# Optimization experiments

Measured on AMD Instinct MI355X. Metric: run time of the kernel, lower is better.

The kernel has to match this reference:

```python
import jax, jax.numpy as jnp
import numpy as np

N = 50000   # nodes per graph
D = 256     # embedding dim
E = 800000  # edges per graph
NEG_SLOPE = 0.2
EPS = 1e-9


def gat_layer(h, src, dst, W, a):
    # SpGraphAttentionLayer: transform, edge attention exp(-leakyrelu(a.[h_i||h_j])),
    # softmax-normalized scatter aggregation, ELU activation.
    h = h @ W                                   # [N, D]
    # a.[h_src || h_dst] == (h @ a[:D])[src] + (h @ a[D:])[dst]  (avoids [E,2D] concat)
    alpha_src = h @ a[:D]                       # [N]
    alpha_dst = h @ a[D:]                       # [N]
    logits = alpha_src[src] + alpha_dst[dst]    # [E]
    e = jnp.exp(-jax.nn.leaky_relu(logits, NEG_SLOPE))  # [E], pyGAT sparse form
    rowsum = jax.ops.segment_sum(e, src, num_segments=N)            # [N]
    num = jax.ops.segment_sum(e[:, None] * h[dst], src, num_segments=N)  # [N, D]
    out = num / (rowsum[:, None] + EPS)
    return jax.nn.elu(out)


def setup_inputs() -> dict:
    key = jax.random.key(0)
    ks = jax.random.split(key, 8)
    w_std = float(np.sqrt(2.0 / (D + D)))  # xavier
    sr_emb = jax.random.normal(ks[0], (N, D), jnp.float32) * w_std
    tg_emb = jax.random.normal(ks[1], (N, D), jnp.float32) * w_std
    W1 = jax.random.normal(ks[2], (D, D), jnp.float32) * w_std
    a1 = jax.random.normal(ks[3], (2 * D,), jnp.float32) * 0.1
    W2 = jax.random.normal(ks[4], (D, D), jnp.float32) * w_std
    a2 = jax.random.normal(ks[5], (2 * D,), jnp.float32) * 0.1
    adj_sr = jax.random.randint(ks[6], (2, E), 0, N, dtype=jnp.int64)
    adj_tg = jax.random.randint(ks[7], (2, E), 0, N, dtype=jnp.int64)
    return {"sr_emb": sr_emb, "tg_emb": tg_emb, "W1": W1, "a1": a1,
            "W2": W2, "a2": a2, "adj_sr": adj_sr, "adj_tg": adj_tg}


def reference(sr_emb, tg_emb, W1, a1, W2, a2, adj_sr, adj_tg):
    # layers are shared across the two graphs (same ModuleList applied to both)
    src_s, dst_s = adj_sr[0], adj_sr[1]
    src_t, dst_t = adj_tg[0], adj_tg[1]
    for (W, a) in ((W1, a1), (W2, a2)):
        sr_emb = gat_layer(sr_emb, src_s, dst_s, W, a)
        tg_emb = gat_layer(tg_emb, src_t, dst_t, W, a)
    return (sr_emb, tg_emb)
```

## Files before the change

kernel.cpp:

```cpp
#include <hip/hip_runtime.h>

#define NEG_SLOPE 0.2f
#define EPS_ 1e-9f

typedef __attribute__((ext_vector_type(8))) short short8v;
typedef __attribute__((ext_vector_type(4))) float f32x4;

__device__ __forceinline__ float bf2f(unsigned short u) {
    return __uint_as_float(((unsigned)u) << 16);
}
__device__ __forceinline__ unsigned short f2bf(float f) {
    unsigned u = __float_as_uint(f);
    u = u + 0x7FFFu + ((u >> 16) & 1u);
    return (unsigned short)(u >> 16);
}

__global__ void hist_kernel(const int* __restrict__ src, int* __restrict__ cnt, int E) {
    int i = blockIdx.x * blockDim.x + threadIdx.x;
    if (i < E) atomicAdd(&cnt[src[i]], 1);
}

__global__ __launch_bounds__(256) void scan1_kernel(const int* __restrict__ cnt,
        int* __restrict__ locpre, int* __restrict__ blocksum, int n) {
    int t = threadIdx.x;
    int lane = t & 63, wid = t >> 6;
    int base = blockIdx.x * 1024 + t * 4;
    int4 v = {0, 0, 0, 0};
    if (base + 3 < n) {
        v = *(const int4*)(cnt + base);
    } else {
        if (base + 0 < n) v.x = cnt[base + 0];
        if (base + 1 < n) v.y = cnt[base + 1];
        if (base + 2 < n) v.z = cnt[base + 2];
        if (base + 3 < n) v.w = cnt[base + 3];
    }
    int s = v.x + v.y + v.z + v.w;
    int incl = s;
    for (int off = 1; off < 64; off <<= 1) {
        int u = __shfl_up(incl, off);
        if (lane >= off) incl += u;
    }
    __shared__ int ws[4];
    if (lane == 63) ws[wid] = incl;
    __syncthreads();
    int woff = 0;
    for (int i = 0; i < wid; ++i) woff += ws[i];
    int excl = incl - s + woff;
    int4 o;
    o.x = excl; o.y = excl + v.x; o.z = o.y + v.y; o.w = o.z + v.z;
    if (base + 3 < n) {
        *(int4*)(locpre + base) = o;
    } else {
        if (base + 0 < n) locpre[base + 0] = o.x;
        if (base + 1 < n) locpre[base + 1] = o.y;
        if (base + 2 < n) locpre[base + 2] = o.z;
        if (base + 3 < n) locpre[base + 3] = o.w;
    }
    if (t == 255) blocksum[blockIdx.x] = excl + s;
}

__global__ __launch_bounds__(64) void scan2_kernel(int* __restrict__ blocksum, int nb,
        int* __restrict__ totout) {
    int lane = threadIdx.x;
    int carry = 0;
    for (int base = 0; base < nb; base += 64) {
        int v = (base + lane < nb) ? blocksum[base + lane] : 0;
        int incl = v;
        for (int off = 1; off < 64; off <<= 1) {
            int u = __shfl_up(incl, off);
            if (lane >= off) incl += u;
        }
        int tot = __shfl(incl, 63);
        if (base + lane < nb) blocksum[base + lane] = incl - v + carry;
        carry += tot;
    }
    if (lane == 0) *totout = carry;
}

__global__ __launch_bounds__(256) void scan3_kernel(const int* __restrict__ locpre,
        const int* __restrict__ blocksum, int* __restrict__ row_ptr,
        int* __restrict__ cursor, int n) {
    int base = blockIdx.x * 1024 + threadIdx.x * 4;
    int off = blocksum[blockIdx.x];
    if (base + 3 < n) {
        int4 v = *(const int4*)(locpre + base);
        v.x += off; v.y += off; v.z += off; v.w += off;
        *(int4*)(row_ptr + base) = v;
        *(int4*)(cursor + base) = v;
    } else {
        for (int i = 0; i < 4; ++i) {
            if (base + i < n) {
                int v = locpre[base + i] + off;
                row_ptr[base + i] = v;
                cursor[base + i] = v;
            }
        }
    }
}

__global__ void scatter_kernel(const int* __restrict__ src, const int* __restrict__ dst,
        int* __restrict__ cursor, int* __restrict__ colv, int* __restrict__ srce, int E) {
    int i = blockIdx.x * blockDim.x + threadIdx.x;
    if (i < E) {
        int s = src[i];
        int p = atomicAdd(&cursor[s], 1);
        colv[p] = dst[i];
        srce[p] = s;
    }
}

__global__ __launch_bounds__(256) void ew_kernel(const int* __restrict__ srce,
        const int* __restrict__ colv, const float* __restrict__ asrc,
        const float* __restrict__ adst, int2* __restrict__ ewc, int E) {
    int i = blockIdx.x * blockDim.x + threadIdx.x;
    if (i < E) {
        int d = colv[i];
        float x = asrc[srce[i]] + adst[d];
        float lr = fmaxf(x, NEG_SLOPE * x);
        ewc[i] = make_int2(d, __float_as_int(__expf(-lr)));
    }
}

__global__ void wt_kernel(const float* __restrict__ W, short* __restrict__ Wt) {
    int nn = blockIdx.x, k = threadIdx.x;
    Wt[nn * 256 + k] = (short)f2bf(W[k * 256 + nn]);
}

template<bool IN_BF16>
__global__ __launch_bounds__(256) void gemm_kernel(const void* __restrict__ hin,
        const short* __restrict__ Wt, unsigned short* __restrict__ hpS,
        const float* __restrict__ af, float* __restrict__ asrc,
        float* __restrict__ adst, int M) {
    __shared__ short As[64 * 40];
    __shared__ short Bt[256 * 40];
    int tid = threadIdx.x;
    int lane = tid & 63, w = tid >> 6;
    int m0 = blockIdx.x * 64;
    size_t Ns = (size_t)M * 32;

    f32x4 acc[16];
#pragma unroll
    for (int t = 0; t < 16; ++t) acc[t] = (f32x4){0.f, 0.f, 0.f, 0.f};

    int ar = tid >> 2;
    int ac = (tid & 3) * 8;
    int agrow = m0 + ar;

    for (int kk = 0; kk < 256; kk += 32) {
        short8v av = (short8v){0,0,0,0,0,0,0,0};
        if constexpr (IN_BF16) {
            if (agrow < M)
                av = *(const short8v*)((const short*)hin + (size_t)agrow * 256 + kk + ac);
        } else {
            if (agrow < M) {
                const float* s = (const float*)hin + (size_t)agrow * 256 + kk + ac;
                float4 v0 = *(const float4*)s;
                float4 v1 = *(const float4*)(s + 4);
                av[0] = (short)f2bf(v0.x); av[1] = (short)f2bf(v0.y);
                av[2] = (short)f2bf(v0.z); av[3] = (short)f2bf(v0.w);
                av[4] = (short)f2bf(v1.x); av[5] = (short)f2bf(v1.y);
                av[6] = (short)f2bf(v1.z); av[7] = (short)f2bf(v1.w);
            }
        }
        *(short8v*)&As[ar * 40 + ac] = av;
        {
            const short* s = Wt + (size_t)tid * 256 + kk;
#pragma unroll
            for (int i = 0; i < 4; ++i)
                *(short8v*)&Bt[tid * 40 + i * 8] = *(const short8v*)(s + i * 8);
        }
        __syncthreads();
        short8v a = *(const short8v*)&As[(16 * w + (lane & 15)) * 40 + (lane >> 4) * 8];
#pragma unroll
        for (int t = 0; t < 16; ++t) {
            short8v b = *(const short8v*)&Bt[(16 * t + (lane & 15)) * 40 + (lane >> 4) * 8];
            acc[t] = __builtin_amdgcn_mfma_f32_16x16x32_bf16(a, b, acc[t], 0, 0, 0);
        }
        __syncthreads();
    }
    int r0 = 16 * w + (lane >> 4) * 4;
    int c0 = lane & 15;
    float a_s[16], a_d[16];
#pragma unroll
    for (int t = 0; t < 16; ++t) {
        a_s[t] = af[16 * t + c0];
        a_d[t] = af[256 + 16 * t + c0];
    }
#pragma unroll
    for (int j = 0; j < 4; ++j) {
        int grow = m0 + r0 + j;
        float ssrc = 0.f, sdst = 0.f;
#pragma unroll
        for (int t = 0; t < 16; ++t) {
            float cv = acc[t][j];
            ssrc = fmaf(cv, a_s[t], ssrc);
            sdst = fmaf(cv, a_d[t], sdst);
            int col = 16 * t + c0;
            if (grow < M)
                hpS[(size_t)(col >> 5) * Ns + (size_t)grow * 32 + (col & 31)] = f2bf(cv);
        }
        for (int off = 1; off < 16; off <<= 1) {
            ssrc += __shfl_xor(ssrc, off);
            sdst += __shfl_xor(sdst, off);
        }
        if (c0 == 0 && grow < M) { asrc[grow] = ssrc; adst[grow] = sdst; }
    }
}

#define EWLD(pp, kk) int2 pp = ewc[min(e + kk, last)];
#define GA(qq, pp)   uint2 qq = *(const uint2*)(base + (size_t)(unsigned)pp.x * 32 + c4);
#define WSEL(ww, pp, kk) float ww = (kk < m) ? __int_as_float(pp.y) : 0.f;
#define ACC(qq, ww) { \
    acc0 = fmaf(ww, __uint_as_float(qq.x << 16), acc0); \
    acc1 = fmaf(ww, __uint_as_float(qq.x & 0xFFFF0000u), acc1); \
    acc2 = fmaf(ww, __uint_as_float(qq.y << 16), acc2); \
    acc3 = fmaf(ww, __uint_as_float(qq.y & 0xFFFF0000u), acc3); \
    rs += ww; }

template<bool OUT_BF16>
__global__ __launch_bounds__(256) void aggregate_kernel(const int* __restrict__ row_ptr,
        const int2* __restrict__ ewc, const unsigned short* __restrict__ hpS,
        void* __restrict__ outp, int n) {
    int bid = blockIdx.x;
    int slice = bid & 7;
    int wid = threadIdx.x >> 6;
    int lane = threadIdx.x & 63;
    int node = (bid >> 3) * 32 + wid * 8 + (lane >> 3);
    int c4 = (lane & 7) * 4;
    bool valid = node < n;
    int nd = valid ? node : 0;
    int beg = row_ptr[nd];
    int end = valid ? row_ptr[nd + 1] : beg;
    int last = end - 1;
    const unsigned short* __restrict__ base = hpS + (size_t)slice * ((size_t)n * 32);
    float acc0 = 0.f, acc1 = 0.f, acc2 = 0.f, acc3 = 0.f, rs = 0.f;
    for (int e = beg; e < end; e += 8) {
        int m = end - e;
        EWLD(p0, 0) EWLD(p1, 1) EWLD(p2, 2) EWLD(p3, 3)
        EWLD(p4, 4) EWLD(p5, 5) EWLD(p6, 6) EWLD(p7, 7)
        GA(q0, p0) GA(q1, p1) GA(q2, p2) GA(q3, p3)
        GA(q4, p4) GA(q5, p5) GA(q6, p6) GA(q7, p7)
        WSEL(w0, p0, 0) WSEL(w1, p1, 1) WSEL(w2, p2, 2) WSEL(w3, p3, 3)
        WSEL(w4, p4, 4) WSEL(w5, p5, 5) WSEL(w6, p6, 6) WSEL(w7, p7, 7)
        ACC(q0, w0) ACC(q1, w1) ACC(q2, w2) ACC(q3, w3)
        ACC(q4, w4) ACC(q5, w5) ACC(q6, w6) ACC(q7, w7)
    }
    if (valid) {
        float inv = 1.f / (rs + EPS_);
        float v0 = acc0 * inv, v1 = acc1 * inv, v2 = acc2 * inv, v3 = acc3 * inv;
        v0 = v0 > 0.f ? v0 : __expf(v0) - 1.f;
        v1 = v1 > 0.f ? v1 : __expf(v1) - 1.f;
        v2 = v2 > 0.f ? v2 : __expf(v2) - 1.f;
        v3 = v3 > 0.f ? v3 : __expf(v3) - 1.f;
        size_t o = (size_t)node * 256 + slice * 32 + c4;
        if constexpr (OUT_BF16) {
            ushort4 ov;
            ov.x = f2bf(v0); ov.y = f2bf(v1); ov.z = f2bf(v2); ov.w = f2bf(v3);
            *(ushort4*)((unsigned short*)outp + o) = ov;
        } else {
            float4 ov = {v0, v1, v2, v3};
            *(float4*)((float*)outp + o) = ov;
        }
    }
}

extern "C" void kernel_launch(void* const* d_in, const int* in_sizes, int n_in,
                              void* d_out, int out_size, void* d_ws, size_t ws_size,
                              hipStream_t stream) {
    const float* sr_emb = (const float*)d_in[0];
    const float* tg_emb = (const float*)d_in[1];
    const float* W1 = (const float*)d_in[2];
    const float* a1 = (const float*)d_in[3];
    const float* W2 = (const float*)d_in[4];
    const float* a2 = (const float*)d_in[5];
    const int* adj_sr = (const int*)d_in[6];
    const int* adj_tg = (const int*)d_in[7];
    int N = in_sizes[0] / 256;
    int E = in_sizes[6] / 2;

    char* p = (char*)d_ws;
    auto alloc = [&](size_t bytes) -> void* {
        void* r = (void*)p;
        p += (bytes + 255) & ~(size_t)255;
        return r;
    };
    int nb = (N + 1023) / 1024;
    int* cnt      = (int*)alloc((size_t)N * 4);
    int* row_ptr  = (int*)alloc((size_t)(N + 1) * 4);
    int* cursor   = (int*)alloc((size_t)N * 4);
    int* locpre   = (int*)alloc((size_t)N * 4);
    int* blocksum = (int*)alloc((size_t)nb * 4);
    int* colv     = (int*)alloc((size_t)(E + 16) * 4);
    int* srce     = (int*)alloc((size_t)(E + 16) * 4);
    int2* ewc     = (int2*)alloc((size_t)(E + 16) * 8);
    short* Wt1    = (short*)alloc(256 * 256 * 2);
    short* Wt2    = (short*)alloc(256 * 256 * 2);
    unsigned short* hpS = (unsigned short*)alloc((size_t)N * 256 * 2);
    float* asrc   = (float*)alloc((size_t)N * 4);
    float* adst   = (float*)alloc((size_t)N * 4);
    short* tmp    = (short*)alloc((size_t)N * 256 * 2);

    wt_kernel<<<256, 256, 0, stream>>>(W1, Wt1);
    wt_kernel<<<256, 256, 0, stream>>>(W2, Wt2);

    int gemm_grid = (N + 63) / 64;
    int agg_grid = 8 * ((N + 31) / 32);
    int e_grid = (E + 255) / 256;

    for (int g = 0; g < 2; ++g) {
        const int* srcv = (g == 0 ? adj_sr : adj_tg);
        const int* dstv = srcv + E;
        const float* emb = (g == 0 ? sr_emb : tg_emb);
        float* outg = (float*)d_out + (size_t)g * N * 256;

        hipMemsetAsync(cnt, 0, (size_t)N * 4, stream);
        hist_kernel<<<e_grid, 256, 0, stream>>>(srcv, cnt, E);
        scan1_kernel<<<nb, 256, 0, stream>>>(cnt, locpre, blocksum, N);
        scan2_kernel<<<1, 64, 0, stream>>>(blocksum, nb, row_ptr + N);
        scan3_kernel<<<nb, 256, 0, stream>>>(locpre, blocksum, row_ptr, cursor, N);
        scatter_kernel<<<e_grid, 256, 0, stream>>>(srcv, dstv, cursor, colv, srce, E);

        gemm_kernel<false><<<gemm_grid, 256, 0, stream>>>(emb, Wt1, hpS, a1, asrc, adst, N);
        ew_kernel<<<e_grid, 256, 0, stream>>>(srce, colv, asrc, adst, ewc, E);
        aggregate_kernel<true><<<agg_grid, 256, 0, stream>>>(row_ptr, ewc, hpS, tmp, N);
        gemm_kernel<true><<<gemm_grid, 256, 0, stream>>>(tmp, Wt2, hpS, a2, asrc, adst, N);
        ew_kernel<<<e_grid, 256, 0, stream>>>(srce, colv, asrc, adst, ewc, E);
        aggregate_kernel<false><<<agg_grid, 256, 0, stream>>>(row_ptr, ewc, hpS, outg, N);
    }
}
```

Measured before the change: 671.8 us.

## Batch both graphs per launch, fuse edge weights into aggregation, split alpha

Processes both graphs in each kernel launch via a grid dimension, which halves the launch count and fills the GPU better. Edge attention weights are computed inside the aggregation from colv, asrc and adst, so the separate ew_kernel and its int2 edge buffer (and srce) are gone. The GEMM is rewritten to stage half of W in LDS once and hold the A fragments in registers, and the alpha dot-products move to a separate kernel that rereads hpS. The layer-1 output is stored as fp32 in the output buffer rather than a bf16 temporary, which adds memory traffic, and the bf16 exp work now repeats per feature slice.

```diff
diff --git a/kernel.cpp b/kernel.cpp
--- a/kernel.cpp
+++ b/kernel.cpp
@@ -15,24 +15,32 @@
     return (unsigned short)(u >> 16);
 }
 
-__global__ void hist_kernel(const int* __restrict__ src, int* __restrict__ cnt, int E) {
+__global__ void hist_kernel(const int* __restrict__ srcA, const int* __restrict__ srcB,
+        int* __restrict__ cnt, int E, int n) {
+    int g = blockIdx.y;
+    const int* src = g ? srcB : srcA;
+    int* c = cnt + (size_t)g * n;
     int i = blockIdx.x * blockDim.x + threadIdx.x;
-    if (i < E) atomicAdd(&cnt[src[i]], 1);
+    if (i < E) atomicAdd(&c[src[i]], 1);
 }
 
 __global__ __launch_bounds__(256) void scan1_kernel(const int* __restrict__ cnt,
-        int* __restrict__ locpre, int* __restrict__ blocksum, int n) {
+        int* __restrict__ locpre, int* __restrict__ blocksum, int n, int nb) {
+    int g = blockIdx.y;
+    const int* cg = cnt + (size_t)g * n;
+    int* lg = locpre + (size_t)g * n;
+    int* bs = blocksum + (size_t)g * nb;
     int t = threadIdx.x;
     int lane = t & 63, wid = t >> 6;
     int base = blockIdx.x * 1024 + t * 4;
     int4 v = {0, 0, 0, 0};
     if (base + 3 < n) {
-        v = *(const int4*)(cnt + base);
+        v = *(const int4*)(cg + base);
     } else {
-        if (base + 0 < n) v.x = cnt[base + 0];
-        if (base + 1 < n) v.y = cnt[base + 1];
-        if (base + 2 < n) v.z = cnt[base + 2];
-        if (base + 3 < n) v.w = cnt[base + 3];
+        if (base + 0 < n) v.x = cg[base + 0];
+        if (base + 1 < n) v.y = cg[base + 1];
+        if (base + 2 < n) v.z = cg[base + 2];
+        if (base + 3 < n) v.w = cg[base + 3];
     }
     int s = v.x + v.y + v.z + v.w;
     int incl = s;
@@ -49,75 +57,74 @@
     int4 o;
     o.x = excl; o.y = excl + v.x; o.z = o.y + v.y; o.w = o.z + v.z;
     if (base + 3 < n) {
-        *(int4*)(locpre + base) = o;
+        *(int4*)(lg + base) = o;
     } else {
-        if (base + 0 < n) locpre[base + 0] = o.x;
-        if (base + 1 < n) locpre[base + 1] = o.y;
-        if (base + 2 < n) locpre[base + 2] = o.z;
-        if (base + 3 < n) locpre[base + 3] = o.w;
-    }
-    if (t == 255) blocksum[blockIdx.x] = excl + s;
+        if (base + 0 < n) lg[base + 0] = o.x;
+        if (base + 1 < n) lg[base + 1] = o.y;
+        if (base + 2 < n) lg[base + 2] = o.z;
+        if (base + 3 < n) lg[base + 3] = o.w;
+    }
+    if (t == 255) bs[blockIdx.x] = excl + s;
 }
 
 __global__ __launch_bounds__(64) void scan2_kernel(int* __restrict__ blocksum, int nb,
-        int* __restrict__ totout) {
+        int* __restrict__ row_ptr, int n) {
+    int g = blockIdx.y;
+    int* bs = blocksum + (size_t)g * nb;
     int lane = threadIdx.x;
     int carry = 0;
     for (int base = 0; base < nb; base += 64) {
-        int v = (base + lane < nb) ? blocksum[base + lane] : 0;
+        int v = (base + lane < nb) ? bs[base + lane] : 0;
         int incl = v;
         for (int off = 1; off < 64; off <<= 1) {
             int u = __shfl_up(incl, off);
             if (lane >= off) incl += u;
         }
         int tot = __shfl(incl, 63);
-        if (base + lane < nb) blocksum[base + lane] = incl - v + carry;
+        if (base + lane < nb) bs[base + lane] = incl - v + carry;
         carry += tot;
     }
-    if (lane == 0) *totout = carry;
+    if (lane == 0) row_ptr[(size_t)g * (n + 1) + n] = carry;
 }
 
 __global__ __launch_bounds__(256) void scan3_kernel(const int* __restrict__ locpre,
         const int* __restrict__ blocksum, int* __restrict__ row_ptr,
-        int* __restrict__ cursor, int n) {
+        int* __restrict__ cursor, int n, int nb) {
+    int g = blockIdx.y;
+    const int* lg = locpre + (size_t)g * n;
+    const int* bs = blocksum + (size_t)g * nb;
+    int* rp = row_ptr + (size_t)g * (n + 1);
+    int* cu = cursor + (size_t)g * n;
     int base = blockIdx.x * 1024 + threadIdx.x * 4;
-    int off = blocksum[blockIdx.x];
+    int off = bs[blockIdx.x];
     if (base + 3 < n) {
-        int4 v = *(const int4*)(locpre + base);
+        int4 v = *(const int4*)(lg + base);
         v.x += off; v.y += off; v.z += off; v.w += off;
-        *(int4*)(row_ptr + base) = v;
-        *(int4*)(cursor + base) = v;
+        *(int4*)(rp + base) = v;
+        *(int4*)(cu + base) = v;
     } else {
         for (int i = 0; i < 4; ++i) {
             if (base + i < n) {
-                int v = locpre[base + i] + off;
-                row_ptr[base + i] = v;
-                cursor[base + i] = v;
+                int v = lg[base + i] + off;
+                rp[base + i] = v;
+                cu[base + i] = v;
             }
         }
     }
 }
 
-__global__ void scatter_kernel(const int* __restrict__ src, const int* __restrict__ dst,
-        int* __restrict__ cursor, int* __restrict__ colv, int* __restrict__ srce, int E) {
+__global__ void scatter_kernel(const int* __restrict__ srcA, const int* __restrict__ dstA,
+        const int* __restrict__ srcB, const int* __restrict__ dstB,
+        int* __restrict__ cursor, int* __restrict__ colv, int E, int n, int ecap) {
+    int g = blockIdx.y;
+    const int* src = g ? srcB : srcA;
+    const int* dst = g ? dstB : dstA;
+    int* cu = cursor + (size_t)g * n;
+    int* cv = colv + (size_t)g * ecap;
     int i = blockIdx.x * blockDim.x + threadIdx.x;
     if (i < E) {
-        int s = src[i];
-        int p = atomicAdd(&cursor[s], 1);
-        colv[p] = dst[i];
-        srce[p] = s;
-    }
-}
-
-__global__ __launch_bounds__(256) void ew_kernel(const int* __restrict__ srce,
-        const int* __restrict__ colv, const float* __restrict__ asrc,
-        const float* __restrict__ adst, int2* __restrict__ ewc, int E) {
-    int i = blockIdx.x * blockDim.x + threadIdx.x;
-    if (i < E) {
-        int d = colv[i];
-        float x = asrc[srce[i]] + adst[d];
-        float lr = fmaxf(x, NEG_SLOPE * x);
-        ewc[i] = make_int2(d, __float_as_int(__expf(-lr)));
+        int p = atomicAdd(&cu[src[i]], 1);
+        cv[p] = dst[i];
     }
 }
 
@@ -126,90 +133,137 @@
     Wt[nn * 256 + k] = (short)f2bf(W[k * 256 + nn]);
 }
 
-template<bool IN_BF16>
-__global__ __launch_bounds__(256) void gemm_kernel(const void* __restrict__ hin,
-        const short* __restrict__ Wt, unsigned short* __restrict__ hpS,
-        const float* __restrict__ af, float* __restrict__ asrc,
-        float* __restrict__ adst, int M) {
-    __shared__ short As[64 * 40];
-    __shared__ short Bt[256 * 40];
+__global__ __launch_bounds__(512) void gemm_kernel(const float* __restrict__ hinA,
+        const float* __restrict__ hinB, const short* __restrict__ Wt,
+        unsigned short* __restrict__ hpS_all, int M) {
+    __shared__ short Bt[32768];
     int tid = threadIdx.x;
     int lane = tid & 63, w = tid >> 6;
-    int m0 = blockIdx.x * 64;
+    int ch = blockIdx.y;
+    int g = blockIdx.z;
+    const float* hin = g ? hinB : hinA;
+    unsigned short* hpS = hpS_all + (size_t)g * M * 256;
+
+    {
+        int n = tid >> 2;
+        int kb = (tid & 3) * 64;
+        const short* srcw = Wt + (size_t)(ch * 128 + n) * 256;
+#pragma unroll
+        for (int i = 0; i < 8; ++i) {
+            int k = kb + i * 8;
+            short8v v = *(const short8v*)(srcw + k);
+            *(short8v*)&Bt[((k >> 3) * 128 + n) * 8] = v;
+        }
+    }
+    __syncthreads();
+
+    int row0 = (blockIdx.x * 8 + w) * 16;
+    if (row0 >= M) return;
+
+    const float* Ap = hin + (size_t)(row0 + (lane & 15)) * 256 + (lane >> 4) * 8;
+    short8v af[8];
+#pragma unroll
+    for (int half = 0; half < 2; ++half) {
+        float4 u0[4], u1[4];
+#pragma unroll
+        for (int c = 0; c < 4; ++c) {
+            u0[c] = *(const float4*)(Ap + (half * 4 + c) * 32);
+            u1[c] = *(const float4*)(Ap + (half * 4 + c) * 32 + 4);
+        }
+#pragma unroll
+        for (int c = 0; c < 4; ++c) {
+            short8v a;
+            a[0] = (short)f2bf(u0[c].x); a[1] = (short)f2bf(u0[c].y);
+            a[2] = (short)f2bf(u0[c].z); a[3] = (short)f2bf(u0[c].w);
+            a[4] = (short)f2bf(u1[c].x); a[5] = (short)f2bf(u1[c].y);
+            a[6] = (short)f2bf(u1[c].z); a[7] = (short)f2bf(u1[c].w);
+            af[half * 4 + c] = a;
+        }
+    }
+
+    f32x4 acc[8];
+#pragma unroll
+    for (int t = 0; t < 8; ++t) acc[t] = (f32x4){0.f, 0.f, 0.f, 0.f};
+
+#pragma unroll
+    for (int c = 0; c < 8; ++c) {
+        int kcf = c * 4 + (lane >> 4);
+#pragma unroll
+        for (int t = 0; t < 8; ++t) {
+            short8v b = *(const short8v*)&Bt[(kcf * 128 + t * 16 + (lane & 15)) * 8];
+            acc[t] = __builtin_amdgcn_mfma_f32_16x16x32_bf16(af[c], b, acc[t], 0, 0, 0);
+        }
+    }
+
     size_t Ns = (size_t)M * 32;
-
-    f32x4 acc[16];
-#pragma unroll
-    for (int t = 0; t < 16; ++t) acc[t] = (f32x4){0.f, 0.f, 0.f, 0.f};
-
-    int ar = tid >> 2;
-    int ac = (tid & 3) * 8;
-    int agrow = m0 + ar;
-
-    for (int kk = 0; kk < 256; kk += 32) {
-        short8v av = (short8v){0,0,0,0,0,0,0,0};
-        if constexpr (IN_BF16) {
-            if (agrow < M)
-                av = *(const short8v*)((const short*)hin + (size_t)agrow * 256 + kk + ac);
-        } else {
-            if (agrow < M) {
-                const float* s = (const float*)hin + (size_t)agrow * 256 + kk + ac;
-                float4 v0 = *(const float4*)s;
-                float4 v1 = *(const float4*)(s + 4);
-                av[0] = (short)f2bf(v0.x); av[1] = (short)f2bf(v0.y);
-                av[2] = (short)f2bf(v0.z); av[3] = (short)f2bf(v0.w);
-                av[4] = (short)f2bf(v1.x); av[5] = (short)f2bf(v1.y);
-                av[6] = (short)f2bf(v1.z); av[7] = (short)f2bf(v1.w);
-            }
-        }
-        *(short8v*)&As[ar * 40 + ac] = av;
-        {
-            const short* s = Wt + (size_t)tid * 256 + kk;
-#pragma unroll
-            for (int i = 0; i < 4; ++i)
-                *(short8v*)&Bt[tid * 40 + i * 8] = *(const short8v*)(s + i * 8);
-        }
-        __syncthreads();
-        short8v a = *(const short8v*)&As[(16 * w + (lane & 15)) * 40 + (lane >> 4) * 8];
-#pragma unroll
-        for (int t = 0; t < 16; ++t) {
-            short8v b = *(const short8v*)&Bt[(16 * t + (lane & 15)) * 40 + (lane >> 4) * 8];
-            acc[t] = __builtin_amdgcn_mfma_f32_16x16x32_bf16(a, b, acc[t], 0, 0, 0);
-        }
-        __syncthreads();
-    }
-    int r0 = 16 * w + (lane >> 4) * 4;
-    int c0 = lane & 15;
-    float a_s[16], a_d[16];
-#pragma unroll
-    for (int t = 0; t < 16; ++t) {
-        a_s[t] = af[16 * t + c0];
-        a_d[t] = af[256 + 16 * t + c0];
-    }
-#pragma unroll
-    for (int j = 0; j < 4; ++j) {
-        int grow = m0 + r0 + j;
-        float ssrc = 0.f, sdst = 0.f;
-#pragma unroll
-        for (int t = 0; t < 16; ++t) {
-            float cv = acc[t][j];
-            ssrc = fmaf(cv, a_s[t], ssrc);
-            sdst = fmaf(cv, a_d[t], sdst);
-            int col = 16 * t + c0;
-            if (grow < M)
-                hpS[(size_t)(col >> 5) * Ns + (size_t)grow * 32 + (col & 31)] = f2bf(cv);
-        }
-        for (int off = 1; off < 16; off <<= 1) {
-            ssrc += __shfl_xor(ssrc, off);
-            sdst += __shfl_xor(sdst, off);
-        }
-        if (c0 == 0 && grow < M) { asrc[grow] = ssrc; adst[grow] = sdst; }
-    }
-}
-
-#define EWLD(pp, kk) int2 pp = ewc[min(e + kk, last)];
-#define GA(qq, pp)   uint2 qq = *(const uint2*)(base + (size_t)(unsigned)pp.x * 32 + c4);
-#define WSEL(ww, pp, kk) float ww = (kk < m) ? __int_as_float(pp.y) : 0.f;
+#pragma unroll
+    for (int t = 0; t < 8; ++t) {
+        int col = ch * 128 + t * 16 + (lane & 15);
+        unsigned short* dst = hpS + (size_t)(col >> 5) * Ns + (col & 31);
+#pragma unroll
+        for (int j = 0; j < 4; ++j) {
+            int row = row0 + (lane >> 4) * 4 + j;
+            dst[(size_t)row * 32] = f2bf(acc[t][j]);
+        }
+    }
+}
+
+__global__ __launch_bounds__(256) void alpha_kernel(const unsigned short* __restrict__ hpS,
+        const float* __restrict__ a, float* __restrict__ asrc, float* __restrict__ adst,
+        int n) {
+    int gid = (blockIdx.x * 256 + threadIdx.x) >> 3;
+    int ln8 = threadIdx.x & 7;
+    if (gid >= 2 * n) return;
+    int g = gid >= n;
+    int node = gid - g * n;
+    const unsigned short* base = hpS + (size_t)g * n * 256;
+    float s0 = 0.f, s1 = 0.f;
+#pragma unroll
+    for (int s = 0; s < 8; ++s) {
+        uint2 q = *(const uint2*)(base + (size_t)s * ((size_t)n * 32)
+                                  + (size_t)node * 32 + ln8 * 4);
+        float f0 = __uint_as_float(q.x << 16);
+        float f1 = __uint_as_float(q.x & 0xFFFF0000u);
+        float f2 = __uint_as_float(q.y << 16);
+        float f3 = __uint_as_float(q.y & 0xFFFF0000u);
+        int ax = s * 32 + ln8 * 4;
+        s0 += f0 * a[ax] + f1 * a[ax + 1] + f2 * a[ax + 2] + f3 * a[ax + 3];
+        s1 += f0 * a[256 + ax] + f1 * a[257 + ax] + f2 * a[258 + ax] + f3 * a[259 + ax];
+    }
+    for (int off = 1; off < 8; off <<= 1) {
+        s0 += __shfl_xor(s0, off);
+        s1 += __shfl_xor(s1, off);
+    }
+    if (ln8 == 0) { asrc[gid] = s0; adst[gid] = s1; }
+}
+
+__global__ __launch_bounds__(256) void aggregate_kernel(const int* __restrict__ row_ptr,
+        const int* __restrict__ colv, const float* __restrict__ asrc,
+        const float* __restrict__ adst, const unsigned short* __restrict__ hpS,
+        float* __restrict__ outp, int n, int ecap) {
+    int slice = blockIdx.x & 7;
+    int ngrp = blockIdx.x >> 3;
+    int g = blockIdx.y;
+    int wid = threadIdx.x >> 6, lane = threadIdx.x & 63;
+    int node = ngrp * 32 + wid * 8 + (lane >> 3);
+    int c4 = (lane & 7) * 4;
+    bool valid = node < n;
+    int nd = valid ? node : 0;
+    const int* rp = row_ptr + (size_t)g * (n + 1);
+    int beg = rp[nd];
+    int end = valid ? rp[nd + 1] : beg;
+    int last = end - 1;
+    const int* cv = colv + (size_t)g * ecap;
+    const float* ad = adst + (size_t)g * n;
+    float ai = asrc[(size_t)g * n + nd];
+    const unsigned short* base = hpS + (size_t)g * n * 256 + (size_t)slice * ((size_t)n * 32);
+
+    float acc0 = 0.f, acc1 = 0.f, acc2 = 0.f, acc3 = 0.f, rs = 0.f;
+#define JLD(jj, kk) int jj = cv[min(e + kk, last)];
+#define DGA(dd, jj) float dd = ad[jj];
+#define HGA(qq, jj) uint2 qq = *(const uint2*)(base + (size_t)(unsigned)jj * 32 + c4);
+#define WCMP(ww, dd, kk) float ww; { float x_ = ai + dd; \
+    ww = (kk < m) ? __expf(-fmaxf(x_, NEG_SLOPE * x_)) : 0.f; }
 #define ACC(qq, ww) { \
     acc0 = fmaf(ww, __uint_as_float(qq.x << 16), acc0); \
     acc1 = fmaf(ww, __uint_as_float(qq.x & 0xFFFF0000u), acc1); \
@@ -217,31 +271,16 @@
     acc3 = fmaf(ww, __uint_as_float(qq.y & 0xFFFF0000u), acc3); \
     rs += ww; }
 
-template<bool OUT_BF16>
-__global__ __launch_bounds__(256) void aggregate_kernel(const int* __restrict__ row_ptr,
-        const int2* __restrict__ ewc, const unsigned short* __restrict__ hpS,
-        void* __restrict__ outp, int n) {
-    int bid = blockIdx.x;
-    int slice = bid & 7;
-    int wid = threadIdx.x >> 6;
-    int lane = threadIdx.x & 63;
-    int node = (bid >> 3) * 32 + wid * 8 + (lane >> 3);
-    int c4 = (lane & 7) * 4;
-    bool valid = node < n;
-    int nd = valid ? node : 0;
-    int beg = row_ptr[nd];
-    int end = valid ? row_ptr[nd + 1] : beg;
-    int last = end - 1;
-    const unsigned short* __restrict__ base = hpS + (size_t)slice * ((size_t)n * 32);
-    float acc0 = 0.f, acc1 = 0.f, acc2 = 0.f, acc3 = 0.f, rs = 0.f;
     for (int e = beg; e < end; e += 8) {
         int m = end - e;
-        EWLD(p0, 0) EWLD(p1, 1) EWLD(p2, 2) EWLD(p3, 3)
-        EWLD(p4, 4) EWLD(p5, 5) EWLD(p6, 6) EWLD(p7, 7)
-        GA(q0, p0) GA(q1, p1) GA(q2, p2) GA(q3, p3)
-        GA(q4, p4) GA(q5, p5) GA(q6, p6) GA(q7, p7)
-        WSEL(w0, p0, 0) WSEL(w1, p1, 1) WSEL(w2, p2, 2) WSEL(w3, p3, 3)
-        WSEL(w4, p4, 4) WSEL(w5, p5, 5) WSEL(w6, p6, 6) WSEL(w7, p7, 7)
+        JLD(j0, 0) JLD(j1, 1) JLD(j2, 2) JLD(j3, 3)
+        JLD(j4, 4) JLD(j5, 5) JLD(j6, 6) JLD(j7, 7)
+        DGA(d0, j0) DGA(d1, j1) DGA(d2, j2) DGA(d3, j3)
+        DGA(d4, j4) DGA(d5, j5) DGA(d6, j6) DGA(d7, j7)
+        HGA(q0, j0) HGA(q1, j1) HGA(q2, j2) HGA(q3, j3)
+        HGA(q4, j4) HGA(q5, j5) HGA(q6, j6) HGA(q7, j7)
+        WCMP(w0, d0, 0) WCMP(w1, d1, 1) WCMP(w2, d2, 2) WCMP(w3, d3, 3)
+        WCMP(w4, d4, 4) WCMP(w5, d5, 5) WCMP(w6, d6, 6) WCMP(w7, d7, 7)
         ACC(q0, w0) ACC(q1, w1) ACC(q2, w2) ACC(q3, w3)
         ACC(q4, w4) ACC(q5, w5) ACC(q6, w6) ACC(q7, w7)
     }
@@ -252,15 +291,8 @@
         v1 = v1 > 0.f ? v1 : __expf(v1) - 1.f;
         v2 = v2 > 0.f ? v2 : __expf(v2) - 1.f;
         v3 = v3 > 0.f ? v3 : __expf(v3) - 1.f;
-        size_t o = (size_t)node * 256 + slice * 32 + c4;
-        if constexpr (OUT_BF16) {
-            ushort4 ov;
-            ov.x = f2bf(v0); ov.y = f2bf(v1); ov.z = f2bf(v2); ov.w = f2bf(v3);
-            *(ushort4*)((unsigned short*)outp + o) = ov;
-        } else {
-            float4 ov = {v0, v1, v2, v3};
-            *(float4*)((float*)outp + o) = ov;
-        }
+        float4 ov = {v0, v1, v2, v3};
+        *(float4*)(outp + (size_t)g * n * 256 + (size_t)node * 256 + slice * 32 + c4) = ov;
     }
 }
 
@@ -285,46 +317,42 @@
         return r;
     };
     int nb = (N + 1023) / 1024;
-    int* cnt      = (int*)alloc((size_t)N * 4);
-    int* row_ptr  = (int*)alloc((size_t)(N + 1) * 4);
-    int* cursor   = (int*)alloc((size_t)N * 4);
-    int* locpre   = (int*)alloc((size_t)N * 4);
-    int* blocksum = (int*)alloc((size_t)nb * 4);
-    int* colv     = (int*)alloc((size_t)(E + 16) * 4);
-    int* srce     = (int*)alloc((size_t)(E + 16) * 4);
-    int2* ewc     = (int2*)alloc((size_t)(E + 16) * 8);
+    int ecap = E + 8;
+    int* cnt      = (int*)alloc((size_t)2 * N * 4);
+    int* row_ptr  = (int*)alloc((size_t)2 * (N + 1) * 4);
+    int* cursor   = (int*)alloc((size_t)2 * N * 4);
+    int* locpre   = (int*)alloc((size_t)2 * N * 4);
+    int* blocksum = (int*)alloc((size_t)2 * nb * 4);
+    int* colv     = (int*)alloc((size_t)2 * ecap * 4);
     short* Wt1    = (short*)alloc(256 * 256 * 2);
     short* Wt2    = (short*)alloc(256 * 256 * 2);
-    unsigned short* hpS = (unsigned short*)alloc((size_t)N * 256 * 2);
-    float* asrc   = (float*)alloc((size_t)N * 4);
-    float* adst   = (float*)alloc((size_t)N * 4);
-    short* tmp    = (short*)alloc((size_t)N * 256 * 2);
-
+    unsigned short* hpS = (unsigned short*)alloc((size_t)2 * N * 256 * 2);
+    float* asrc   = (float*)alloc((size_t)2 * N * 4);
+    float* adst   = (float*)alloc((size_t)2 * N * 4);
+    float* outf   = (float*)d_out;
+
+    hipMemsetAsync(cnt, 0, (size_t)2 * N * 4, stream);
     wt_kernel<<<256, 256, 0, stream>>>(W1, Wt1);
     wt_kernel<<<256, 256, 0, stream>>>(W2, Wt2);
-
-    int gemm_grid = (N + 63) / 64;
-    int agg_grid = 8 * ((N + 31) / 32);
     int e_grid = (E + 255) / 256;
-
-    for (int g = 0; g < 2; ++g) {
-        const int* srcv = (g == 0 ? adj_sr : adj_tg);
-        const int* dstv = srcv + E;
-        const float* emb = (g == 0 ? sr_emb : tg_emb);
-        float* outg = (float*)d_out + (size_t)g * N * 256;
-
-        hipMemsetAsync(cnt, 0, (size_t)N * 4, stream);
-        hist_kernel<<<e_grid, 256, 0, stream>>>(srcv, cnt, E);
-        scan1_kernel<<<nb, 256, 0, stream>>>(cnt, locpre, blocksum, N);
-        scan2_kernel<<<1, 64, 0, stream>>>(blocksum, nb, row_ptr + N);
-        scan3_kernel<<<nb, 256, 0, stream>>>(locpre, blocksum, row_ptr, cursor, N);
-        scatter_kernel<<<e_grid, 256, 0, stream>>>(srcv, dstv, cursor, colv, srce, E);
-
-        gemm_kernel<false><<<gemm_grid, 256, 0, stream>>>(emb, Wt1, hpS, a1, asrc, adst, N);
-        ew_kernel<<<e_grid, 256, 0, stream>>>(srce, colv, asrc, adst, ewc, E);
-        aggregate_kernel<true><<<agg_grid, 256, 0, stream>>>(row_ptr, ewc, hpS, tmp, N);
-        gemm_kernel<true><<<gemm_grid, 256, 0, stream>>>(tmp, Wt2, hpS, a2, asrc, adst, N);
-        ew_kernel<<<e_grid, 256, 0, stream>>>(srce, colv, asrc, adst, ewc, E);
-        aggregate_kernel<false><<<agg_grid, 256, 0, stream>>>(row_ptr, ewc, hpS, outg, N);
-    }
-}
+    hist_kernel<<<dim3(e_grid, 2), 256, 0, stream>>>(adj_sr, adj_tg, cnt, E, N);
+    scan1_kernel<<<dim3(nb, 2), 256, 0, stream>>>(cnt, locpre, blocksum, N, nb);
+    scan2_kernel<<<dim3(1, 2), 64, 0, stream>>>(blocksum, nb, row_ptr, N);
+    scan3_kernel<<<dim3(nb, 2), 256, 0, stream>>>(locpre, blocksum, row_ptr, cursor, N, nb);
+    scatter_kernel<<<dim3(e_grid, 2), 256, 0, stream>>>(adj_sr, adj_sr + E,
+            adj_tg, adj_tg + E, cursor, colv, E, N, ecap);
+
+    int gemm_rt = (N + 127) / 128;
+    int alpha_grid = (2 * N + 31) / 32;
+    int agg_gx = 8 * ((N + 31) / 32);
+
+    gemm_kernel<<<dim3(gemm_rt, 2, 2), 512, 0, stream>>>(sr_emb, tg_emb, Wt1, hpS, N);
+    alpha_kernel<<<alpha_grid, 256, 0, stream>>>(hpS, a1, asrc, adst, N);
+    aggregate_kernel<<<dim3(agg_gx, 2), 256, 0, stream>>>(row_ptr, colv, asrc, adst,
+            hpS, outf, N, ecap);
+    gemm_kernel<<<dim3(gemm_rt, 2, 2), 512, 0, stream>>>(outf, outf + (size_t)N * 256,
+            Wt2, hpS, N);
+    alpha_kernel<<<alpha_grid, 256, 0, stream>>>(hpS, a2, asrc, adst, N);
+    aggregate_kernel<<<dim3(agg_gx, 2), 256, 0, stream>>>(row_ptr, colv, asrc, adst,
+            hpS, outf, N, ecap);
+}
```

Result: faster. 636.1 us (-5.3%).
